# Performance work log

Measured on AMD Instinct MI355X. Metric: run time of the kernel, lower is better.

The kernel has to match this reference:

```python
import jax, jax.numpy as jnp
import numpy as np

B, T, EI, EO = 64, 512, 1024, 1024

def setup_inputs() -> dict:
    key = jax.random.key(0)
    k1, k2, k3, k4 = jax.random.split(key, 4)
    x = jax.random.normal(k1, (B, T, EI), dtype=jnp.float32)
    h0 = jax.random.normal(k2, (B, EO), dtype=jnp.float32)
    # match nn.Linear init scale roughly (uniform +-1/sqrt(fan_in))
    wxh = jax.random.uniform(k3, (EI, EO), dtype=jnp.float32, minval=-1.0, maxval=1.0) / np.sqrt(EI)
    whf = jax.random.uniform(k4, (EO, EO), dtype=jnp.float32, minval=-1.0, maxval=1.0) / np.sqrt(EO)
    return {"x": x, "h0": h0, "wxh": wxh, "whf": whf}

def reference(x, h0, wxh, whf):
    # Minimal GRU (all NOT_MUTATED flags = 1.0):
    #   ft = sigmoid(h_{t-1} @ whf); gt = tanh(x_t @ wxh)
    #   h_t = (1 - ft) * h_{t-1} + ft * gt; out_t = h_t
    def step(h, xt):
        ft = jax.nn.sigmoid(h @ whf)          # [B, EO]
        gt = jnp.tanh(xt @ wxh)               # [B, EO]
        h = (1.0 - ft) * h + ft * gt
        return h, h
    xT = jnp.swapaxes(x, 0, 1)                # [T, B, EI]
    hT, outs = jax.lax.scan(step, h0, xT)     # outs: [T, B, EO]
    outs = jnp.swapaxes(outs, 0, 1)           # [B, T, EO]
    return outs, hT
```

## Files before the change

### kernel.cpp

```cpp
#include <hip/hip_runtime.h>
#include <stdint.h>

#define B_   64
#define T_   512
#define EI_  1024
#define EO_  1024

typedef __attribute__((ext_vector_type(4))) float  f32x4;
typedef __attribute__((ext_vector_type(8))) short  s16x8;
typedef __attribute__((ext_vector_type(4))) unsigned short u16x4;
typedef unsigned long long u64;

__device__ __forceinline__ unsigned short f2bf(float f) {
    union { float f; unsigned int u; } v; v.f = f;
    unsigned int r = v.u + 0x7FFFu + ((v.u >> 16) & 1u);
    return (unsigned short)(r >> 16);
}

__global__ void prep_kernel(const float* __restrict__ wxh, const float* __restrict__ whf,
                            const float* __restrict__ h0,
                            unsigned short* __restrict__ wxhT, unsigned short* __restrict__ whfT,
                            unsigned short* __restrict__ hbf,
                            unsigned int* __restrict__ flags)
{
    __shared__ unsigned short Ts[64][72];
    const int bid = blockIdx.x;
    const float* src = (bid & 1) ? whf : wxh;
    unsigned short* dst = (bid & 1) ? whfT : wxhT;
    const int tile = bid >> 1;
    const int k0 = (tile >> 4) * 64, n0 = (tile & 15) * 64;
    const int tid = threadIdx.x;

    #pragma unroll
    for (int it = 0; it < 4; ++it) {
        int r  = it * 16 + (tid >> 4);
        int cq = tid & 15;
        f32x4 v = *(const f32x4*)(src + (size_t)(k0 + r) * EO_ + n0 + cq * 4);
        #pragma unroll
        for (int i = 0; i < 4; ++i) Ts[cq * 4 + i][r] = f2bf(v[i]);
    }
    __syncthreads();
    #pragma unroll
    for (int it = 0; it < 2; ++it) {
        int n = it * 32 + (tid >> 3);
        int c = tid & 7;
        s16x8 v = *(const s16x8*)(&Ts[n][c * 8]);
        *(s16x8*)(dst + (size_t)(n0 + n) * EI_ + k0 + c * 8) = v;
    }
    if (bid < 256) {
        int idx = bid * 256 + tid;
        hbf[65536 + idx] = f2bf(h0[idx]);
    }
    if (bid == 0) flags[tid] = 0u;
}

__launch_bounds__(256, 2)
__global__ void gemm_g_kernel(const float* __restrict__ X,
                              const unsigned short* __restrict__ WT,
                              float* __restrict__ out)
{
    __shared__ alignas(16) unsigned short As[128 * 72];
    __shared__ alignas(16) unsigned short Bs[128 * 72];

    const int bid = blockIdx.x;
    const int bn = bid & 7, bm = bid >> 3;
    const int m0 = bm * 128, n0 = bn * 128;
    const int tid  = threadIdx.x;
    const int lane = tid & 63, w = tid >> 6;
    const int wr = w >> 1, wc = w & 1;
    const int l15 = lane & 15, lg = lane >> 4;

    f32x4 acc[4][4] = {};

    for (int kt = 0; kt < EI_ / 64; ++kt) {
        const int k0 = kt * 64;
        #pragma unroll
        for (int p = 0; p < 8; ++p) {
            int row = p * 16 + (tid >> 4);
            int kq  = tid & 15;
            f32x4 v = *(const f32x4*)(X + (size_t)(m0 + row) * EI_ + k0 + kq * 4);
            u16x4 hv4;
            hv4[0] = f2bf(v[0]); hv4[1] = f2bf(v[1]); hv4[2] = f2bf(v[2]); hv4[3] = f2bf(v[3]);
            *(u16x4*)(&As[row * 72 + kq * 4]) = hv4;
        }
        #pragma unroll
        for (int p = 0; p < 4; ++p) {
            int n  = p * 32 + (tid >> 3);
            int kq = tid & 7;
            s16x8 v = *(const s16x8*)(WT + (size_t)(n0 + n) * EI_ + k0 + kq * 8);
            *(s16x8*)(&Bs[n * 72 + kq * 8]) = v;
        }
        __syncthreads();
        #pragma unroll
        for (int kk = 0; kk < 2; ++kk) {
            s16x8 a[4], b[4];
            #pragma unroll
            for (int mt = 0; mt < 4; ++mt)
                a[mt] = *(const s16x8*)(&As[(wr * 64 + mt * 16 + l15) * 72 + kk * 32 + lg * 8]);
            #pragma unroll
            for (int nt = 0; nt < 4; ++nt)
                b[nt] = *(const s16x8*)(&Bs[(wc * 64 + nt * 16 + l15) * 72 + kk * 32 + lg * 8]);
            #pragma unroll
            for (int mt = 0; mt < 4; ++mt)
                #pragma unroll
                for (int nt = 0; nt < 4; ++nt)
                    acc[mt][nt] = __builtin_amdgcn_mfma_f32_16x16x32_bf16(a[mt], b[nt], acc[mt][nt], 0, 0, 0);
        }
        __syncthreads();
    }
    #pragma unroll
    for (int mt = 0; mt < 4; ++mt) {
        #pragma unroll
        for (int nt = 0; nt < 4; ++nt) {
            #pragma unroll
            for (int r = 0; r < 4; ++r) {
                int row = wr * 64 + mt * 16 + lg * 4 + r;
                int col = wc * 64 + nt * 16 + l15;
                float s = acc[mt][nt][r];
                float e = __expf(2.f * s);
                out[(size_t)(m0 + row) * EO_ + n0 + col] = 1.f - 2.f / (e + 1.f);
            }
        }
    }
}

__launch_bounds__(256, 1)
__global__ void recur_kernel(const float* __restrict__ h0,
                             const unsigned short* __restrict__ whfT,
                             unsigned short* hbf,
                             unsigned int* flags,
                             float* out)
{
    const int j = blockIdx.x;
    const int tid = threadIdx.x;
    const int lane = tid & 63;
    const int g = tid >> 6;
    const int l15 = lane & 15, lg = lane >> 4;

    s16x8 Wf[32];
    #pragma unroll
    for (int kk = 0; kk < 32; ++kk)
        Wf[kk] = *(const s16x8*)(whfT + (size_t)(j * 16 + l15) * EO_ + kk * 32 + lg * 8);
    #pragma unroll
    for (int kk = 0; kk < 32; ++kk)
        asm volatile("" : "+v"(Wf[kk]));

    const int row = g * 16 + l15;
    const int c0  = j * 16 + lg * 4;
    float h[4];
    {
        f32x4 v = *(const f32x4*)(h0 + (size_t)row * EO_ + c0);
        h[0] = v[0]; h[1] = v[1]; h[2] = v[2]; h[3] = v[3];
    }
    unsigned int* const flg = flags + g * 64;

    for (int t = 0; t < T_; ++t) {
        f32x4 gv = *(const f32x4*)(out + ((size_t)row * T_ + t) * EO_ + c0);

        const unsigned int want = (unsigned int)t;
        int spins = 0;
        for (;;) {
            unsigned int f = __hip_atomic_load(&flg[lane], __ATOMIC_RELAXED,
                                               __HIP_MEMORY_SCOPE_AGENT);
            if (__ballot(f >= want) == ~0ULL) break;
            if (++spins > (1 << 20)) break;
        }

        asm volatile("s_waitcnt vmcnt(0)" ::: "memory");
        __builtin_amdgcn_sched_barrier(0);

        const char* aptr = (const char*)(hbf + (size_t)((t & 1) ^ 1) * 65536
                                         + (size_t)(g * 16 + l15) * 1024 + lg * 8);
        f32x4 ab[32];
#define CLD(OFF) asm volatile("global_load_dwordx4 %0, %1, off offset:" #OFF " sc0 sc1" \
                              : "=v"(ab[(OFF) / 64]) : "v"(aptr) : "memory")
        CLD(0);    CLD(64);   CLD(128);  CLD(192);  CLD(256);  CLD(320);  CLD(384);  CLD(448);
        CLD(512);  CLD(576);  CLD(640);  CLD(704);  CLD(768);  CLD(832);  CLD(896);  CLD(960);
        CLD(1024); CLD(1088); CLD(1152); CLD(1216); CLD(1280); CLD(1344); CLD(1408); CLD(1472);
        CLD(1536); CLD(1600); CLD(1664); CLD(1728); CLD(1792); CLD(1856); CLD(1920); CLD(1984);
#undef CLD

        f32x4 acc[4] = {};
        asm volatile("s_waitcnt vmcnt(24)" ::: "memory");
        __builtin_amdgcn_sched_barrier(0);
        #pragma unroll
        for (int kk = 0; kk < 8; ++kk) {
            union { f32x4 f; s16x8 s; } a_; a_.f = ab[kk];
            acc[kk & 3] = __builtin_amdgcn_mfma_f32_16x16x32_bf16(Wf[kk], a_.s, acc[kk & 3], 0, 0, 0);
        }
        asm volatile("s_waitcnt vmcnt(16)" ::: "memory");
        __builtin_amdgcn_sched_barrier(0);
        #pragma unroll
        for (int kk = 8; kk < 16; ++kk) {
            union { f32x4 f; s16x8 s; } a_; a_.f = ab[kk];
            acc[kk & 3] = __builtin_amdgcn_mfma_f32_16x16x32_bf16(Wf[kk], a_.s, acc[kk & 3], 0, 0, 0);
        }
        asm volatile("s_waitcnt vmcnt(8)" ::: "memory");
        __builtin_amdgcn_sched_barrier(0);
        #pragma unroll
        for (int kk = 16; kk < 24; ++kk) {
            union { f32x4 f; s16x8 s; } a_; a_.f = ab[kk];
            acc[kk & 3] = __builtin_amdgcn_mfma_f32_16x16x32_bf16(Wf[kk], a_.s, acc[kk & 3], 0, 0, 0);
        }
        asm volatile("s_waitcnt vmcnt(0)" ::: "memory");
        __builtin_amdgcn_sched_barrier(0);
        #pragma unroll
        for (int kk = 24; kk < 32; ++kk) {
            union { f32x4 f; s16x8 s; } a_; a_.f = ab[kk];
            acc[kk & 3] = __builtin_amdgcn_mfma_f32_16x16x32_bf16(Wf[kk], a_.s, acc[kk & 3], 0, 0, 0);
        }

        f32x4 ho;
        #pragma unroll
        for (int r = 0; r < 4; ++r) {
            float s = acc[0][r] + acc[1][r] + acc[2][r] + acc[3][r];
            float fg = 1.f / (1.f + __expf(-s));
            h[r] = (1.f - fg) * h[r] + fg * gv[r];
            ho[r] = h[r];
        }

        u64 pk = (u64)f2bf(h[0]) | ((u64)f2bf(h[1]) << 16)
               | ((u64)f2bf(h[2]) << 32) | ((u64)f2bf(h[3]) << 48);
        __hip_atomic_store((u64*)(hbf + (size_t)(t & 1) * 65536 + (size_t)row * 1024 + c0),
                           pk, __ATOMIC_RELAXED, __HIP_MEMORY_SCOPE_AGENT);
        asm volatile("s_waitcnt vmcnt(0)" ::: "memory");
        if (lane == 0)
            __hip_atomic_store(&flg[j], (unsigned int)(t + 1),
                               __ATOMIC_RELAXED, __HIP_MEMORY_SCOPE_AGENT);

        *(f32x4*)(out + ((size_t)row * T_ + t) * EO_ + c0) = ho;
    }

    f32x4 hf; hf[0] = h[0]; hf[1] = h[1]; hf[2] = h[2]; hf[3] = h[3];
    *(f32x4*)(out + (size_t)B_ * T_ * EO_ + (size_t)row * EO_ + c0) = hf;
}

extern "C" void kernel_launch(void* const* d_in, const int* in_sizes, int n_in,
                              void* d_out, int out_size, void* d_ws, size_t ws_size,
                              hipStream_t stream)
{
    const float* x   = (const float*)d_in[0];
    const float* h0  = (const float*)d_in[1];
    const float* wxh = (const float*)d_in[2];
    const float* whf = (const float*)d_in[3];
    float* out = (float*)d_out;

    char* ws = (char*)d_ws;
    unsigned short* whfT  = (unsigned short*)(ws);
    unsigned short* wxhT  = (unsigned short*)(ws + (size_t)2 * 1024 * 1024);
    unsigned short* hbf   = (unsigned short*)(ws + (size_t)4 * 1024 * 1024);
    unsigned int*   flags = (unsigned int*)  (ws + (size_t)4 * 1024 * 1024 + 256 * 1024);

    prep_kernel<<<512, 256, 0, stream>>>(wxh, whf, h0, wxhT, whfT, hbf, flags);
    gemm_g_kernel<<<2048, 256, 0, stream>>>(x, wxhT, out);
    recur_kernel<<<64, 256, 0, stream>>>(h0, whfT, hbf, flags, out);
}
```

Baseline: 4.090 ms.

## Split recurrence flag wait per half and remap GEMM block order

The recurrent kernel now waits on the first 32 producer flags, issues loads for the first half of h, then waits on the remaining flags before loading the second half. The aim is to overlap h loads with the wait for slower producers. The staged vmcnt waits between MFMA groups are replaced by one full wait. The GEMM block index is also permuted so consecutive blocks share the same weight column tile, which may improve cache locality. The flag polling now uses a one-iteration-stale value, which could add an extra poll round.

After: 4.387 ms, median of 4. 1.07x slower.

```diff
diff --git a/kernel.cpp b/kernel.cpp
--- a/kernel.cpp
+++ b/kernel.cpp
@@ -62,7 +62,7 @@
     __shared__ alignas(16) unsigned short As[128 * 72];
     __shared__ alignas(16) unsigned short Bs[128 * 72];
 
-    const int bid = blockIdx.x;
+    const int bid = (blockIdx.x & 7) * 256 + (blockIdx.x >> 3);
     const int bn = bid & 7, bm = bid >> 3;
     const int m0 = bm * 128, n0 = bn * 128;
     const int tid  = threadIdx.x;
@@ -125,11 +125,11 @@
 }
 
 __launch_bounds__(256, 1)
-__global__ void recur_kernel(const float* __restrict__ h0,
-                             const unsigned short* __restrict__ whfT,
-                             unsigned short* hbf,
-                             unsigned int* flags,
-                             float* out)
+__global__ void recur_k(const float* __restrict__ h0,
+                        const unsigned short* __restrict__ whfT,
+                        unsigned short* hbf,
+                        unsigned int* flags,
+                        float* out)
 {
     const int j = blockIdx.x;
     const int tid = threadIdx.x;
@@ -158,40 +158,49 @@
         f32x4 gv = *(const f32x4*)(out + ((size_t)row * T_ + t) * EO_ + c0);
 
         const unsigned int want = (unsigned int)t;
-        int spins = 0;
-        for (;;) {
-            unsigned int f = __hip_atomic_load(&flg[lane], __ATOMIC_RELAXED,
-                                               __HIP_MEMORY_SCOPE_AGENT);
-            if (__ballot(f >= want) == ~0ULL) break;
-            if (++spins > (1 << 20)) break;
-        }
-
-        asm volatile("s_waitcnt vmcnt(0)" ::: "memory");
-        __builtin_amdgcn_sched_barrier(0);
-
         const char* aptr = (const char*)(hbf + (size_t)((t & 1) ^ 1) * 65536
-                                         + (size_t)(g * 16 + l15) * 1024 + lg * 8);
+                                         + (size_t)row * 1024 + lg * 8);
         f32x4 ab[32];
+
+        {
+            unsigned int fA = __hip_atomic_load(&flg[lane], __ATOMIC_RELAXED,
+                                                __HIP_MEMORY_SCOPE_AGENT);
+            int spins = 0;
+            for (;;) {
+                unsigned int fB = __hip_atomic_load(&flg[lane], __ATOMIC_RELAXED,
+                                                    __HIP_MEMORY_SCOPE_AGENT);
+                if (__ballot(lane >= 32 || fA >= want) == ~0ULL) break;
+                fA = fB;
+                if (++spins > (1 << 20)) break;
+            }
+        }
+        __builtin_amdgcn_sched_barrier(0);
 #define CLD(OFF) asm volatile("global_load_dwordx4 %0, %1, off offset:" #OFF " sc0 sc1" \
-                              : "=v"(ab[(OFF) / 64]) : "v"(aptr) : "memory")
+                              : "=&v"(ab[(OFF) / 64]) : "v"(aptr) : "memory")
         CLD(0);    CLD(64);   CLD(128);  CLD(192);  CLD(256);  CLD(320);  CLD(384);  CLD(448);
         CLD(512);  CLD(576);  CLD(640);  CLD(704);  CLD(768);  CLD(832);  CLD(896);  CLD(960);
+
+        {
+            unsigned int fA = __hip_atomic_load(&flg[lane], __ATOMIC_RELAXED,
+                                                __HIP_MEMORY_SCOPE_AGENT);
+            int spins = 0;
+            for (;;) {
+                unsigned int fB = __hip_atomic_load(&flg[lane], __ATOMIC_RELAXED,
+                                                    __HIP_MEMORY_SCOPE_AGENT);
+                if (__ballot(lane < 32 || fA >= want) == ~0ULL) break;
+                fA = fB;
+                if (++spins > (1 << 20)) break;
+            }
+        }
+        asm volatile("s_waitcnt vmcnt(0)" ::: "memory");
+        __builtin_amdgcn_sched_barrier(0);
         CLD(1024); CLD(1088); CLD(1152); CLD(1216); CLD(1280); CLD(1344); CLD(1408); CLD(1472);
         CLD(1536); CLD(1600); CLD(1664); CLD(1728); CLD(1792); CLD(1856); CLD(1920); CLD(1984);
 #undef CLD
 
         f32x4 acc[4] = {};
-        asm volatile("s_waitcnt vmcnt(24)" ::: "memory");
-        __builtin_amdgcn_sched_barrier(0);
-        #pragma unroll
-        for (int kk = 0; kk < 8; ++kk) {
-            union { f32x4 f; s16x8 s; } a_; a_.f = ab[kk];
-            acc[kk & 3] = __builtin_amdgcn_mfma_f32_16x16x32_bf16(Wf[kk], a_.s, acc[kk & 3], 0, 0, 0);
-        }
-        asm volatile("s_waitcnt vmcnt(16)" ::: "memory");
-        __builtin_amdgcn_sched_barrier(0);
-        #pragma unroll
-        for (int kk = 8; kk < 16; ++kk) {
+        #pragma unroll
+        for (int kk = 0; kk < 16; ++kk) {
             union { f32x4 f; s16x8 s; } a_; a_.f = ab[kk];
             acc[kk & 3] = __builtin_amdgcn_mfma_f32_16x16x32_bf16(Wf[kk], a_.s, acc[kk & 3], 0, 0, 0);
         }
@@ -253,5 +262,5 @@
 
     prep_kernel<<<512, 256, 0, stream>>>(wxh, whf, h0, wxhT, whfT, hbf, flags);
     gemm_g_kernel<<<2048, 256, 0, stream>>>(x, wxhT, out);
-    recur_kernel<<<64, 256, 0, stream>>>(h0, whfT, hbf, flags, out);
-}
+    recur_k<<<64, 256, 0, stream>>>(h0, whfT, hbf, flags, out);
+}
```
